# Kernel tuning notes

Measured on AMD Instinct MI355X. Metric: run time of the kernel, lower is better.

## Reference

```python
import jax, jax.numpy as jnp
import numpy as np

B, N, D = 16, 1369, 1024
HID, NH = 512, 8
SCALE = np.sqrt(D // NH)


def _pos_encoding_2d(n, d):
    ps = int(np.sqrt(n))  # 37; n is a perfect square here
    div = jnp.exp(jnp.arange(0, d // 2, 2, dtype=jnp.float32) * (-np.log(10000.0) / (d // 2)))
    rows = (jnp.arange(n) // ps).astype(jnp.float32)
    cols = (jnp.arange(n) % ps).astype(jnp.float32)
    def interleave(s, c):
        return jnp.stack([s, c], axis=-1).reshape(n, -1)
    half_row = interleave(jnp.sin(rows[:, None] * div), jnp.cos(rows[:, None] * div))
    half_col = interleave(jnp.sin(cols[:, None] * div), jnp.cos(cols[:, None] * div))
    return jnp.concatenate([half_row, half_col], axis=-1)  # [n, d]


def _center_bias(n, strength=0.3):
    ps = int(np.sqrt(n))
    c = ps // 2
    y, x = jnp.meshgrid(jnp.arange(ps, dtype=jnp.float32), jnp.arange(ps, dtype=jnp.float32), indexing='ij')
    d2 = (x - c) ** 2 + (y - c) ** 2
    sigma = ps / 6.0
    return (jnp.exp(-d2 / (2.0 * sigma ** 2)).reshape(-1)) * strength  # [n]


def setup_inputs() -> dict:
    key = jax.random.key(0)
    ks = jax.random.split(key, 16)
    s = 0.02
    return {
        'patch_tokens': jax.random.normal(ks[0], (B, N, D), dtype=jnp.float32),
        'curiosity_score': jax.random.uniform(ks[1], (B,), dtype=jnp.float32),
        'Wq': jax.random.normal(ks[2], (D, D), dtype=jnp.float32) * s,
        'bq': jax.random.uniform(ks[3], (D,), minval=-0.05, maxval=0.05, dtype=jnp.float32),
        'Wk': jax.random.normal(ks[4], (D, D), dtype=jnp.float32) * s,
        'bk': jax.random.uniform(ks[5], (D,), minval=-0.05, maxval=0.05, dtype=jnp.float32),
        'Wv': jax.random.normal(ks[6], (D, D), dtype=jnp.float32) * s,
        'bv': jnp.zeros((D,), dtype=jnp.float32),
        'Wc1': jax.random.normal(ks[7], (1, HID // 8), dtype=jnp.float32) * s,
        'bc1': jnp.zeros((HID // 8,), dtype=jnp.float32),
        'Wc2': jax.random.normal(ks[8], (HID // 8, NH), dtype=jnp.float32) * s,
        'bc2': jnp.zeros((NH,), dtype=jnp.float32),
        'Wp1': jax.random.normal(ks[9], (D, HID), dtype=jnp.float32) * s,
        'bp1': jnp.zeros((HID,), dtype=jnp.float32),
        'Wp2': jax.random.normal(ks[10], (HID, HID // 4), dtype=jnp.float32) * s,
        'bp2': jnp.zeros((HID // 4,), dtype=jnp.float32),
        'adaptive_weight': jnp.float32(0.5),
    }


def reference(patch_tokens, curiosity_score, Wq, bq, Wk, bk, Wv, bv,
              Wc1, bc1, Wc2, bc2, Wp1, bp1, Wp2, bp2, adaptive_weight):
    b, n, d = patch_tokens.shape
    x = patch_tokens + _pos_encoding_2d(n, d)[None]  # [B,N,D]

    q = x @ Wq + bq
    k = x @ Wk + bk
    v = x @ Wv + bv

    scores = jnp.einsum('bqd,bkd->bqk', q, k) / SCALE          # [B,N,N]
    attn = jax.nn.softmax(scores, axis=-1)                     # dropout p=0 / eval
    attended = jnp.einsum('bqk,bkd->bqd', attn, v)             # [B,N,D]

    cb = _center_bias(n)[None]                                 # [1,N]
    VAR_EPS = 1e-6

    pa = attn.mean(axis=1) + cb
    # fallback chain (data-dependent in torch; expressed with jnp.where)
    pa2 = jnp.diagonal(attn, axis1=-2, axis2=-1) + cb
    pa = jnp.where(jnp.var(pa, ddof=1) < VAR_EPS, pa2, pa)
    pa3 = attn.max(axis=-1) + cb
    pa = jnp.where(jnp.var(pa, ddof=1) < VAR_EPS, pa3, pa)
    norms = jnp.linalg.norm(x, axis=-1)
    noise = jax.random.normal(jax.random.key(42), norms.shape, dtype=norms.dtype) * 0.1 * jnp.std(norms, ddof=1)
    pa = jnp.where(jnp.var(pa, ddof=1) < VAR_EPS, norms + noise, pa)

    pa = pa / (pa.sum(axis=-1, keepdims=True) + 1e-8)

    # curiosity modulation
    h = jax.nn.relu(curiosity_score[:, None] @ Wc1 + bc1)
    cm = jax.nn.sigmoid(h @ Wc2 + bc2)                         # [B,NH]
    cw = cm.mean(axis=-1, keepdims=True)                       # [B,1]
    modulated = pa * (1.0 + cw)
    fa = adaptive_weight * modulated + (1.0 - adaptive_weight) * pa

    fa = jnp.clip(fa, 1e-8, None)
    fa = fa / (fa.sum(axis=-1, keepdims=True) + 1e-8)

    weighted = jnp.sum(attended * fa[..., None], axis=1)       # [B,D]
    focal = jax.nn.relu(weighted @ Wp1 + bp1) @ Wp2 + bp2      # [B,HID//4]
    return focal, fa
```

## Files before the change

kernel.cpp:

```cpp
#include <hip/hip_runtime.h>
#include <hip/hip_bf16.h>
#include <cstdint>

#define B_   16
#define N_   1369
#define NP   1536
#define D_   1024
#define NQKV 3072
#define SLD  1568
#define QLD  3104

typedef __bf16 bf16x8_t __attribute__((ext_vector_type(8)));
typedef __bf16 bf16x4_t __attribute__((ext_vector_type(4)));
typedef float  f32x4_t  __attribute__((ext_vector_type(4)));

__device__ __forceinline__ float  bf2f(__bf16 x) { return (float)x; }
__device__ __forceinline__ __bf16 f2bf(float x)  { return (__bf16)x; }

#define GLOAD_LDS16(g, l) __builtin_amdgcn_global_load_lds( \
    (const __attribute__((address_space(1))) void*)(g),     \
    (__attribute__((address_space(3))) void*)(l), 16, 0, 0)

__global__ __launch_bounds__(256)
void pos_kernel(float* __restrict__ pos)
{
    const int idx = blockIdx.x * 256 + threadIdx.x;
    if (idx >= N_ * D_) return;
    const int n = idx >> 10, f = idx & 1023;
    const int row = n / 37, col = n - row * 37;
    const float base = (f < 512) ? (float)row : (float)col;
    const int  t2   = (f & 511) >> 1;
    const float dv  = __expf(-0.03597789207803197f * (float)t2);
    const float ang = base * dv;
    pos[idx] = (f & 1) ? cosf(ang) : sinf(ang);
}

__global__ __launch_bounds__(256)
void addpos_kernel(const float* __restrict__ patch, const float* __restrict__ pos,
                   __bf16* __restrict__ X)
{
    const long tid = (long)blockIdx.x * 256 + threadIdx.x;
    const long e   = tid * 4;
    const int  f   = (int)(e & 1023);
    const long nb  = e >> 10;
    const int  n   = (int)(nb % NP);
    const long b   = nb / NP;
    bf16x4_t o;
    if (n < N_) {
        const float4 p = *(const float4*)(patch + ((b * N_ + n) << 10) + f);
        const float4 q = *(const float4*)(pos + ((long)n << 10) + f);
        o[0] = f2bf(p.x + q.x); o[1] = f2bf(p.y + q.y);
        o[2] = f2bf(p.z + q.z); o[3] = f2bf(p.w + q.w);
    } else {
        o[0] = o[1] = o[2] = o[3] = f2bf(0.f);
    }
    *(bf16x4_t*)(X + e) = o;
}

__global__ __launch_bounds__(256)
void wcast_kernel(const float* __restrict__ W0, const float* __restrict__ W1,
                  const float* __restrict__ W2,
                  __bf16* __restrict__ T0, __bf16* __restrict__ T1, __bf16* __restrict__ T2)
{
    const float* W = blockIdx.z == 0 ? W0 : (blockIdx.z == 1 ? W1 : W2);
    __bf16*      T = blockIdx.z == 0 ? T0 : (blockIdx.z == 1 ? T1 : T2);
    __shared__ float tile[64][65];
    const int o0 = blockIdx.x * 64, i0 = blockIdx.y * 64;
    const int t = threadIdx.x;
    const int tr = t >> 4, tc = (t & 15) * 4;
    #pragma unroll
    for (int rr = 0; rr < 64; rr += 16) {
        float4 v = *(const float4*)(W + (long)(i0 + rr + tr) * 1024 + o0 + tc);
        tile[rr + tr][tc + 0] = v.x; tile[rr + tr][tc + 1] = v.y;
        tile[rr + tr][tc + 2] = v.z; tile[rr + tr][tc + 3] = v.w;
    }
    __syncthreads();
    #pragma unroll
    for (int rr = 0; rr < 64; rr += 16) {
        bf16x4_t o;
        o[0] = f2bf(tile[tc + 0][rr + tr]); o[1] = f2bf(tile[tc + 1][rr + tr]);
        o[2] = f2bf(tile[tc + 2][rr + tr]); o[3] = f2bf(tile[tc + 3][rr + tr]);
        *(bf16x4_t*)(T + (long)(o0 + rr + tr) * 1024 + i0 + tc) = o;
    }
}

__global__ __launch_bounds__(256)
void bcat_kernel(const float* __restrict__ bq, const float* __restrict__ bk,
                 const float* __restrict__ bv, float* __restrict__ bcat)
{
    const int i = blockIdx.x * 256 + threadIdx.x;
    if (i >= NQKV) return;
    const int p = i >> 10, j = i & 1023;
    bcat[i] = p == 0 ? bq[j] : (p == 1 ? bk[j] : bv[j]);
}

template<int HAS_BIAS>
__global__ __launch_bounds__(512, 2)
void gemm256(const __bf16* __restrict__ A, const __bf16* __restrict__ Bt,
             __bf16* __restrict__ C, const float* __restrict__ bias,
             int lda, int ldb, int ldc, int Kd, float scale,
             long sA, long sB, long sC, int tilesN, int tilesPerBatch, int cpx)
{
    __shared__ __bf16 lds[65536];
    const int bid = blockIdx.x;
    const int vt  = (bid & 7) * cpx + (bid >> 3);
    const int bz  = vt / tilesPerBatch;
    const int rem = vt - bz * tilesPerBatch;
    const int ty  = rem / tilesN;
    const int tx  = rem - ty * tilesN;
    A  += (long)bz * sA;  Bt += (long)bz * sB;  C += (long)bz * sC;
    const int m0 = ty * 256, n0 = tx * 256;

    const int t  = threadIdx.x;
    const int w  = t >> 6, l = t & 63;
    const int wr = w >> 2, wc = w & 3;
    const int lr = l & 15, lh = l >> 4;

    const int laneF  = (lr * 64 + ((lh * 16) ^ (((lr >> 3) & 1) << 5))) >> 1;
    const int rstage = w * 16 + (l >> 2);
    const int kstage = ((l & 3) * 8) ^ (((l >> 5) & 1) << 4);

    const __bf16* Ag = A  + (long)(m0 + rstage) * lda + kstage;
    const __bf16* Bg = Bt + (long)(n0 + rstage) * ldb + kstage;
    __bf16* dA = lds + (w * 2) * 512;
    __bf16* dB = lds + 16384 + (w * 2) * 512;

#define SA_(buf, half, kt) do {                                       \
    const __bf16* g_ = Ag + (long)(half) * 128 * lda + (kt) * 64;     \
    __bf16* d_ = dA + (buf) * 32768 + (half) * 8192;                  \
    GLOAD_LDS16(g_, d_); GLOAD_LDS16(g_ + 32, d_ + 512); } while (0)
#define SB_(buf, half, kt) do {                                       \
    const __bf16* g_ = Bg + (long)(half) * 128 * ldb + (kt) * 64;     \
    __bf16* d_ = dB + (buf) * 32768 + (half) * 8192;                  \
    GLOAD_LDS16(g_, d_); GLOAD_LDS16(g_ + 32, d_ + 512); } while (0)

    f32x4_t acc[8][4] = {};
    bf16x8_t bfr[4][2];

#define BREADS_() do { const __bf16* bp_ = lds + cbB + laneF;                              \
    bfr[0][0] = *(const bf16x8_t*)(bp_);        bfr[0][1] = *(const bf16x8_t*)(bp_ + 512); \
    bfr[1][0] = *(const bf16x8_t*)(bp_ + 1024); bfr[1][1] = *(const bf16x8_t*)(bp_ + 1536);\
    bfr[2][0] = *(const bf16x8_t*)(bp_ + 2048); bfr[2][1] = *(const bf16x8_t*)(bp_ + 2560);\
    bfr[3][0] = *(const bf16x8_t*)(bp_ + 3072); bfr[3][1] = *(const bf16x8_t*)(bp_ + 3584);} while (0)

#define PHASE_(p, P0R, STG, VMW) do {                                                  \
    const __bf16* ap_ = lds + cbase + wr * 8192 + (p) * 2048 + laneF;                  \
    bf16x8_t a00 = *(const bf16x8_t*)(ap_);                                            \
    bf16x8_t a01 = *(const bf16x8_t*)(ap_ + 512);                                      \
    bf16x8_t a10 = *(const bf16x8_t*)(ap_ + 1024);                                     \
    bf16x8_t a11 = *(const bf16x8_t*)(ap_ + 1536);                                     \
    P0R;                                                                               \
    STG;                                                                               \
    __builtin_amdgcn_s_barrier();                                                      \
    asm volatile("s_waitcnt lgkmcnt(0)" ::: "memory");                                 \
    __builtin_amdgcn_sched_barrier(0);                                                 \
    __builtin_amdgcn_s_setprio(1);                                                     \
    _Pragma("unroll") for (int nn = 0; nn < 4; ++nn)                                   \
      acc[(p)*2+0][nn] = __builtin_amdgcn_mfma_f32_16x16x32_bf16(a00, bfr[nn][0], acc[(p)*2+0][nn], 0, 0, 0); \
    _Pragma("unroll") for (int nn = 0; nn < 4; ++nn)                                   \
      acc[(p)*2+1][nn] = __builtin_amdgcn_mfma_f32_16x16x32_bf16(a10, bfr[nn][0], acc[(p)*2+1][nn], 0, 0, 0); \
    _Pragma("unroll") for (int nn = 0; nn < 4; ++nn)                                   \
      acc[(p)*2+0][nn] = __builtin_amdgcn_mfma_f32_16x16x32_bf16(a01, bfr[nn][1], acc[(p)*2+0][nn], 0, 0, 0); \
    _Pragma("unroll") for (int nn = 0; nn < 4; ++nn)                                   \
      acc[(p)*2+1][nn] = __builtin_amdgcn_mfma_f32_16x16x32_bf16(a11, bfr[nn][1], acc[(p)*2+1][nn], 0, 0, 0); \
    __builtin_amdgcn_s_setprio(0);                                                     \
    VMW;                                                                               \
    __builtin_amdgcn_s_barrier();                                                      \
  } while (0)

    const int NT = Kd >> 6;
    SA_(0, 0, 0); SA_(0, 1, 0); SB_(0, 0, 0); SB_(0, 1, 0);
    SB_(1, 0, 1); SB_(1, 1, 1);
    asm volatile("s_waitcnt vmcnt(4)" ::: "memory");
    __builtin_amdgcn_s_barrier();

    for (int tk = 0; tk < NT; ++tk) {
        const int c  = tk & 1, o = c ^ 1;
        const int t1 = (tk + 1 < NT) ? tk + 1 : NT - 1;
        const int t2 = (tk + 2 < NT) ? tk + 2 : NT - 1;
        const int cbase = c * 32768;
        const int cbB   = cbase + 16384 + wc * 4096;
        PHASE_(0, BREADS_(), SA_(o, 0, t1), ((void)0));
        PHASE_(1, ((void)0), SA_(o, 1, t1), ((void)0));
        PHASE_(2, ((void)0), SB_(c, 0, t2), ((void)0));
        PHASE_(3, ((void)0), SB_(c, 1, t2),
               asm volatile("s_waitcnt vmcnt(4)" ::: "memory"));
    }

    #pragma unroll
    for (int mi = 0; mi < 8; ++mi) {
        const int row = m0 + wr * 128 + mi * 16 + lh * 4;
        #pragma unroll
        for (int nn = 0; nn < 4; ++nn) {
            const int col = n0 + wc * 64 + nn * 16 + lr;
            const float bb = HAS_BIAS ? bias[col] : 0.0f;
            #pragma unroll
            for (int q = 0; q < 4; ++q)
                C[(long)(row + q) * ldc + col] = f2bf(acc[mi][nn][q] * scale + bb);
        }
    }
#undef SA_
#undef SB_
#undef BREADS_
#undef PHASE_
}

__global__ __launch_bounds__(256)
void softmax_kernel(__bf16* __restrict__ S)
{
    const int wid  = threadIdx.x >> 6;
    const int lane = threadIdx.x & 63;
    const int q    = blockIdx.x * 4 + wid;
    const int b    = blockIdx.y;
    if (q >= N_) return;
    __bf16* row = S + ((long)b * NP + q) * SLD;
    float v[24];
    float m = -1e30f;
    #pragma unroll
    for (int j = 0; j < 3; ++j) {
        const int k0 = j * 512 + lane * 8;
        bf16x8_t raw = *(const bf16x8_t*)(row + k0);
        #pragma unroll
        for (int i = 0; i < 8; ++i) {
            const float x = (k0 + i < N_) ? bf2f(raw[i]) : -1e30f;
            v[j * 8 + i] = x; m = fmaxf(m, x);
        }
    }
    #pragma unroll
    for (int o = 32; o; o >>= 1) m = fmaxf(m, __shfl_xor(m, o));
    float s = 0.f;
    #pragma unroll
    for (int j = 0; j < 3; ++j) {
        const int k0 = j * 512 + lane * 8;
        #pragma unroll
        for (int i = 0; i < 8; ++i) {
            if (k0 + i < N_) { const float e = __expf(v[j * 8 + i] - m); v[j * 8 + i] = e; s += e; }
            else             v[j * 8 + i] = 0.f;
        }
    }
    #pragma unroll
    for (int o = 32; o; o >>= 1) s += __shfl_xor(s, o);
    const float inv = 1.f / s;
    #pragma unroll
    for (int j = 0; j < 3; ++j) {
        const int k0 = j * 512 + lane * 8;
        bf16x8_t o8;
        #pragma unroll
        for (int i = 0; i < 8; ++i) o8[i] = f2bf(v[j * 8 + i] * inv);
        *(bf16x8_t*)(row + k0) = o8;
    }
}

template<int WEIGHTED>
__global__ __launch_bounds__(256)
void colsum_kernel(const __bf16* __restrict__ attn, const float* __restrict__ wv,
                   float* __restrict__ out)
{
    const int t = threadIdx.x;
    if (t >= 192) return;
    const int b  = blockIdx.y;
    const int q0 = blockIdx.x * 16;
    const int q1 = (q0 + 16 < N_) ? q0 + 16 : N_;
    const int k8 = t * 8;
    float s[8] = {};
    const __bf16* base = attn + (long)b * NP * SLD + k8;
    for (int q = q0; q < q1; ++q) {
        bf16x8_t v = *(const bf16x8_t*)(base + (long)q * SLD);
        const float wq = WEIGHTED ? wv[b * NP + q] : 1.0f;
        #pragma unroll
        for (int i = 0; i < 8; ++i) s[i] += wq * bf2f(v[i]);
    }
    #pragma unroll
    for (int i = 0; i < 8; ++i) atomicAdd(out + b * NP + k8 + i, s[i]);
}

__global__ __launch_bounds__(256)
void fa_kernel(const float* __restrict__ pa_raw, const float* __restrict__ curiosity,
               const float* __restrict__ Wc1, const float* __restrict__ bc1,
               const float* __restrict__ Wc2, const float* __restrict__ bc2,
               const float* __restrict__ aw_p,
               float* __restrict__ fa_ws, float* __restrict__ out_fa)
{
    const int b = blockIdx.x, t = threadIdx.x;
    __shared__ float hsh[64];
    __shared__ float red[8];
    __shared__ float cwsh;
    if (t < 64) hsh[t] = fmaxf(0.f, curiosity[b] * Wc1[t] + bc1[t]);
    __syncthreads();
    if (t < 8) {
        float a = bc2[t];
        for (int j = 0; j < 64; ++j) a += hsh[j] * Wc2[j * 8 + t];
        red[t] = 1.f / (1.f + __expf(-a));
    }
    __syncthreads();
    if (t == 0) {
        float cw = 0.f;
        for (int i = 0; i < 8; ++i) cw += red[i];
        cwsh = cw * 0.125f;
    }
    __syncthreads();
    const float aw   = aw_p[0];
    const float modf = 1.f + aw * cwsh;
    const float sig  = 37.f / 6.f;
    const float inv2s2 = 1.f / (2.f * sig * sig);
    float pv[6];
    float s1 = 0.f;
    #pragma unroll
    for (int i = 0; i < 6; ++i) {
        const int k = t + i * 256;
        float p = 0.f;
        if (k < N_) {
            const int y = k / 37, x = k - y * 37;
            const float d2 = (float)((x - 18) * (x - 18) + (y - 18) * (y - 18));
            const float cb = 0.3f * __expf(-d2 * inv2s2);
            p = pa_raw[b * NP + k] * (1.f / 1369.f) + cb;
        }
        pv[i] = p; s1 += p;
    }
    #pragma unroll
    for (int o = 32; o; o >>= 1) s1 += __shfl_xor(s1, o);
    __syncthreads();
    if (!(t & 63)) red[t >> 6] = s1;
    __syncthreads();
    s1 = red[0] + red[1] + red[2] + red[3];
    const float inv1 = 1.f / (s1 + 1e-8f);
    float s2 = 0.f;
    #pragma unroll
    for (int i = 0; i < 6; ++i) {
        const int k = t + i * 256;
        if (k < N_) {
            const float f = fmaxf(pv[i] * inv1 * modf, 1e-8f);
            pv[i] = f; s2 += f;
        }
    }
    #pragma unroll
    for (int o = 32; o; o >>= 1) s2 += __shfl_xor(s2, o);
    if (!(t & 63)) red[4 + (t >> 6)] = s2;
    __syncthreads();
    s2 = red[4] + red[5] + red[6] + red[7];
    const float inv2 = 1.f / (s2 + 1e-8f);
    #pragma unroll
    for (int i = 0; i < 6; ++i) {
        const int k = t + i * 256;
        if (k < N_) {
            const float f = pv[i] * inv2;
            fa_ws[b * NP + k]  = f;
            out_fa[b * N_ + k] = f;
        }
    }
}

__global__ __launch_bounds__(256)
void weighted_kernel(const float* __restrict__ g, const __bf16* __restrict__ V,
                     int ldv, float* __restrict__ wout)
{
    const int b  = blockIdx.y;
    const int k0 = blockIdx.x * 86;
    const int k1 = (k0 + 86 < N_) ? k0 + 86 : N_;
    const int d  = threadIdx.x * 4;
    float a0 = 0, a1 = 0, a2 = 0, a3 = 0;
    const __bf16* vb = V + (long)b * NP * ldv + d;
    for (int k = k0; k < k1; ++k) {
        const float gv = g[b * NP + k];
        bf16x4_t vv = *(const bf16x4_t*)(vb + (long)k * ldv);
        a0 += gv * bf2f(vv[0]); a1 += gv * bf2f(vv[1]);
        a2 += gv * bf2f(vv[2]); a3 += gv * bf2f(vv[3]);
    }
    atomicAdd(wout + b * D_ + d + 0, a0);
    atomicAdd(wout + b * D_ + d + 1, a1);
    atomicAdd(wout + b * D_ + d + 2, a2);
    atomicAdd(wout + b * D_ + d + 3, a3);
}

__global__ __launch_bounds__(256)
void focal_kernel(const float* __restrict__ weighted, const float* __restrict__ Wp1,
                  const float* __restrict__ bp1, const float* __restrict__ Wp2,
                  const float* __restrict__ bp2, float* __restrict__ out)
{
    const int b = blockIdx.x, t = threadIdx.x;
    __shared__ float wsh[1024];
    __shared__ float hsh[512];
    for (int i = t; i < 1024; i += 256) wsh[i] = weighted[b * 1024 + i];
    __syncthreads();
    for (int j = t; j < 512; j += 256) {
        float a = bp1[j];
        for (int d2 = 0; d2 < 1024; ++d2) a += wsh[d2] * Wp1[d2 * 512 + j];
        hsh[j] = fmaxf(a, 0.f);
    }
    __syncthreads();
    for (int o = t; o < 128; o += 256) {
        float a = bp2[o];
        for (int j = 0; j < 512; ++j) a += hsh[j] * Wp2[j * 128 + o];
        out[b * 128 + o] = a;
    }
}

extern "C" void kernel_launch(void* const* d_in, const int* in_sizes, int n_in,
                              void* d_out, int out_size, void* d_ws, size_t ws_size,
                              hipStream_t stream)
{
    const float* patch     = (const float*)d_in[0];
    const float* curiosity = (const float*)d_in[1];
    const float* Wq  = (const float*)d_in[2];
    const float* bq  = (const float*)d_in[3];
    const float* Wk  = (const float*)d_in[4];
    const float* bk  = (const float*)d_in[5];
    const float* Wv  = (const float*)d_in[6];
    const float* bv  = (const float*)d_in[7];
    const float* Wc1 = (const float*)d_in[8];
    const float* bc1 = (const float*)d_in[9];
    const float* Wc2 = (const float*)d_in[10];
    const float* bc2 = (const float*)d_in[11];
    const float* Wp1 = (const float*)d_in[12];
    const float* bp1 = (const float*)d_in[13];
    const float* Wp2 = (const float*)d_in[14];
    const float* bp2 = (const float*)d_in[15];
    const float* aw  = (const float*)d_in[16];
    float* out = (float*)d_out;

    char* ws = (char*)d_ws;
    size_t off = 0;
    auto alloc = [&](size_t bytes) -> char* {
        char* p = ws + off;
        off += (bytes + 255) & ~(size_t)255;
        return p;
    };
    float*  pos  = (float*) alloc((size_t)N_ * D_ * 4);
    __bf16* X    = (__bf16*)alloc((size_t)B_ * NP * D_ * 2);
    __bf16* WT   = (__bf16*)alloc((size_t)3 * D_ * D_ * 2);
    const size_t S_BYTES = (size_t)B_ * NP * SLD * 2;
    if (off < S_BYTES) off = S_BYTES;
    __bf16* S    = (__bf16*)ws;
    __bf16* QKV  = (__bf16*)alloc((size_t)B_ * NP * QLD * 2);
    float*  pa   = (float*) alloc((size_t)B_ * NP * 4);
    float*  faw  = (float*) alloc((size_t)B_ * NP * 4);
    float*  gbuf = (float*) alloc((size_t)B_ * NP * 4);
    float*  wsum = (float*) alloc((size_t)B_ * D_ * 4);
    float*  bcat = (float*) alloc((size_t)NQKV * 4);

    (void)hipMemsetAsync(pa,   0, (size_t)B_ * NP * 4, stream);
    (void)hipMemsetAsync(gbuf, 0, (size_t)B_ * NP * 4, stream);
    (void)hipMemsetAsync(wsum, 0, (size_t)B_ * D_ * 4, stream);

    pos_kernel<<<(N_ * D_ + 255) / 256, 256, 0, stream>>>(pos);
    addpos_kernel<<<(int)((size_t)B_ * NP * D_ / 4 / 256), 256, 0, stream>>>(patch, pos, X);
    {
        dim3 g(16, 16, 3);
        wcast_kernel<<<g, 256, 0, stream>>>(Wq, Wk, Wv,
                                            WT, WT + D_ * D_, WT + 2 * D_ * D_);
    }
    bcat_kernel<<<(NQKV + 255) / 256, 256, 0, stream>>>(bq, bk, bv, bcat);
    {
        const int nwg = 96 * 12;
        gemm256<1><<<nwg, 512, 0, stream>>>(X, WT, QKV, bcat,
                                            D_, D_, QLD, D_, 1.0f,
                                            0, 0, 0, 12, nwg, nwg / 8);
    }
    {
        const int nwg = 36 * B_;
        gemm256<0><<<nwg, 512, 0, stream>>>(QKV, QKV + D_, S, nullptr,
                                            QLD, QLD, SLD, D_,
                                            0.08838834764831845f,
                                            (long)NP * QLD, (long)NP * QLD,
                                            (long)NP * SLD, 6, 36, nwg / 8);
    }
    {
        dim3 g((N_ + 3) / 4, B_);
        softmax_kernel<<<g, 256, 0, stream>>>(S);
    }
    {
        dim3 g(86, B_);
        colsum_kernel<0><<<g, 256, 0, stream>>>(S, nullptr, pa);
    }
    fa_kernel<<<B_, 256, 0, stream>>>(pa, curiosity, Wc1, bc1, Wc2, bc2, aw,
                                      faw, out + B_ * 128);
    {
        dim3 g(86, B_);
        colsum_kernel<1><<<g, 256, 0, stream>>>(S, faw, gbuf);
    }
    {
        dim3 g(16, B_);
        weighted_kernel<<<g, 256, 0, stream>>>(gbuf, QKV + 2 * D_, QLD, wsum);
    }
    focal_kernel<<<B_, 256, 0, stream>>>(wsum, Wp1, bp1, Wp2, bp2, out);
}
```

Baseline: 599.5 us.

## Software-pipeline LDS fragment reads in GEMM and split focal MLP into parallel kernels

```diff
diff --git a/kernel.cpp b/kernel.cpp
--- a/kernel.cpp
+++ b/kernel.cpp
@@ -122,8 +122,8 @@
 
     const __bf16* Ag = A  + (long)(m0 + rstage) * lda + kstage;
     const __bf16* Bg = Bt + (long)(n0 + rstage) * ldb + kstage;
-    __bf16* dA = lds + (w * 2) * 512;
-    __bf16* dB = lds + 16384 + (w * 2) * 512;
+    __bf16* dA = lds + w * 1024;
+    __bf16* dB = lds + 16384 + w * 1024;
 
 #define SA_(buf, half, kt) do {                                       \
     const __bf16* g_ = Ag + (long)(half) * 128 * lda + (kt) * 64;     \
@@ -136,55 +136,73 @@
 
     f32x4_t acc[8][4] = {};
     bf16x8_t bfr[4][2];
-
-#define BREADS_() do { const __bf16* bp_ = lds + cbB + laneF;                              \
+    bf16x8_t aX0, aX1, aX2, aX3, aY0, aY1, aY2, aY3;
+
+#define AREAD_(S0,S1,S2,S3, base, p) do {                                    \
+    const __bf16* ap_ = lds + (base) + wr * 8192 + (p) * 2048 + laneF;       \
+    S0 = *(const bf16x8_t*)(ap_);                                            \
+    S1 = *(const bf16x8_t*)(ap_ + 512);                                      \
+    S2 = *(const bf16x8_t*)(ap_ + 1024);                                     \
+    S3 = *(const bf16x8_t*)(ap_ + 1536); } while (0)
+
+#define BREAD_(base) do { const __bf16* bp_ = lds + (base) + laneF;                        \
     bfr[0][0] = *(const bf16x8_t*)(bp_);        bfr[0][1] = *(const bf16x8_t*)(bp_ + 512); \
     bfr[1][0] = *(const bf16x8_t*)(bp_ + 1024); bfr[1][1] = *(const bf16x8_t*)(bp_ + 1536);\
     bfr[2][0] = *(const bf16x8_t*)(bp_ + 2048); bfr[2][1] = *(const bf16x8_t*)(bp_ + 2560);\
     bfr[3][0] = *(const bf16x8_t*)(bp_ + 3072); bfr[3][1] = *(const bf16x8_t*)(bp_ + 3584);} while (0)
 
-#define PHASE_(p, P0R, STG, VMW) do {                                                  \
-    const __bf16* ap_ = lds + cbase + wr * 8192 + (p) * 2048 + laneF;                  \
-    bf16x8_t a00 = *(const bf16x8_t*)(ap_);                                            \
-    bf16x8_t a01 = *(const bf16x8_t*)(ap_ + 512);                                      \
-    bf16x8_t a10 = *(const bf16x8_t*)(ap_ + 1024);                                     \
-    bf16x8_t a11 = *(const bf16x8_t*)(ap_ + 1536);                                     \
-    P0R;                                                                               \
-    STG;                                                                               \
-    __builtin_amdgcn_s_barrier();                                                      \
-    asm volatile("s_waitcnt lgkmcnt(0)" ::: "memory");                                 \
-    __builtin_amdgcn_sched_barrier(0);                                                 \
+#define MFMAC_(pp, S0,S1,S2,S3) do {                                                   \
     __builtin_amdgcn_s_setprio(1);                                                     \
     _Pragma("unroll") for (int nn = 0; nn < 4; ++nn)                                   \
-      acc[(p)*2+0][nn] = __builtin_amdgcn_mfma_f32_16x16x32_bf16(a00, bfr[nn][0], acc[(p)*2+0][nn], 0, 0, 0); \
+      acc[(pp)*2+0][nn] = __builtin_amdgcn_mfma_f32_16x16x32_bf16(S0, bfr[nn][0], acc[(pp)*2+0][nn], 0, 0, 0); \
     _Pragma("unroll") for (int nn = 0; nn < 4; ++nn)                                   \
-      acc[(p)*2+1][nn] = __builtin_amdgcn_mfma_f32_16x16x32_bf16(a10, bfr[nn][0], acc[(p)*2+1][nn], 0, 0, 0); \
+      acc[(pp)*2+1][nn] = __builtin_amdgcn_mfma_f32_16x16x32_bf16(S2, bfr[nn][0], acc[(pp)*2+1][nn], 0, 0, 0); \
     _Pragma("unroll") for (int nn = 0; nn < 4; ++nn)                                   \
-      acc[(p)*2+0][nn] = __builtin_amdgcn_mfma_f32_16x16x32_bf16(a01, bfr[nn][1], acc[(p)*2+0][nn], 0, 0, 0); \
+      acc[(pp)*2+0][nn] = __builtin_amdgcn_mfma_f32_16x16x32_bf16(S1, bfr[nn][1], acc[(pp)*2+0][nn], 0, 0, 0); \
     _Pragma("unroll") for (int nn = 0; nn < 4; ++nn)                                   \
-      acc[(p)*2+1][nn] = __builtin_amdgcn_mfma_f32_16x16x32_bf16(a11, bfr[nn][1], acc[(p)*2+1][nn], 0, 0, 0); \
-    __builtin_amdgcn_s_setprio(0);                                                     \
-    VMW;                                                                               \
-    __builtin_amdgcn_s_barrier();                                                      \
-  } while (0)
+      acc[(pp)*2+1][nn] = __builtin_amdgcn_mfma_f32_16x16x32_bf16(S3, bfr[nn][1], acc[(pp)*2+1][nn], 0, 0, 0); \
+    __builtin_amdgcn_s_setprio(0); } while (0)
+
+#define SBAR_ __builtin_amdgcn_sched_barrier(0)
+#define BAR_  __builtin_amdgcn_s_barrier()
 
     const int NT = Kd >> 6;
     SA_(0, 0, 0); SA_(0, 1, 0); SB_(0, 0, 0); SB_(0, 1, 0);
     SB_(1, 0, 1); SB_(1, 1, 1);
     asm volatile("s_waitcnt vmcnt(4)" ::: "memory");
-    __builtin_amdgcn_s_barrier();
+    BAR_;
 
     for (int tk = 0; tk < NT; ++tk) {
         const int c  = tk & 1, o = c ^ 1;
         const int t1 = (tk + 1 < NT) ? tk + 1 : NT - 1;
         const int t2 = (tk + 2 < NT) ? tk + 2 : NT - 1;
+        const int st = (tk + 2 < NT);
         const int cbase = c * 32768;
         const int cbB   = cbase + 16384 + wc * 4096;
-        PHASE_(0, BREADS_(), SA_(o, 0, t1), ((void)0));
-        PHASE_(1, ((void)0), SA_(o, 1, t1), ((void)0));
-        PHASE_(2, ((void)0), SB_(c, 0, t2), ((void)0));
-        PHASE_(3, ((void)0), SB_(c, 1, t2),
-               asm volatile("s_waitcnt vmcnt(4)" ::: "memory"));
+        AREAD_(aX0, aX1, aX2, aX3, cbase, 0);
+        BREAD_(cbB);
+        SBAR_;
+        AREAD_(aY0, aY1, aY2, aY3, cbase, 1);
+        SA_(o, 0, t1);
+        SBAR_; BAR_;
+        MFMAC_(0, aX0, aX1, aX2, aX3);
+        BAR_;
+        AREAD_(aX0, aX1, aX2, aX3, cbase, 2);
+        SA_(o, 1, t1);
+        SBAR_; BAR_;
+        MFMAC_(1, aY0, aY1, aY2, aY3);
+        BAR_;
+        AREAD_(aY0, aY1, aY2, aY3, cbase, 3);
+        SB_(c, 0, t2);
+        SBAR_; BAR_;
+        MFMAC_(2, aX0, aX1, aX2, aX3);
+        BAR_;
+        SB_(c, 1, t2);
+        SBAR_; BAR_;
+        MFMAC_(3, aY0, aY1, aY2, aY3);
+        if (st) { asm volatile("s_waitcnt vmcnt(4)" ::: "memory"); }
+        else    { asm volatile("s_waitcnt vmcnt(0)" ::: "memory"); }
+        BAR_;
     }
 
     #pragma unroll
@@ -201,8 +219,11 @@
     }
 #undef SA_
 #undef SB_
-#undef BREADS_
-#undef PHASE_
+#undef AREAD_
+#undef BREAD_
+#undef MFMAC_
+#undef SBAR_
+#undef BAR_
 }
 
 __global__ __launch_bounds__(256)
@@ -373,26 +394,35 @@
 }
 
 __global__ __launch_bounds__(256)
-void focal_kernel(const float* __restrict__ weighted, const float* __restrict__ Wp1,
-                  const float* __restrict__ bp1, const float* __restrict__ Wp2,
-                  const float* __restrict__ bp2, float* __restrict__ out)
-{
-    const int b = blockIdx.x, t = threadIdx.x;
-    __shared__ float wsh[1024];
-    __shared__ float hsh[512];
-    for (int i = t; i < 1024; i += 256) wsh[i] = weighted[b * 1024 + i];
-    __syncthreads();
-    for (int j = t; j < 512; j += 256) {
-        float a = bp1[j];
-        for (int d2 = 0; d2 < 1024; ++d2) a += wsh[d2] * Wp1[d2 * 512 + j];
-        hsh[j] = fmaxf(a, 0.f);
-    }
-    __syncthreads();
-    for (int o = t; o < 128; o += 256) {
-        float a = bp2[o];
-        for (int j = 0; j < 512; ++j) a += hsh[j] * Wp2[j * 128 + o];
-        out[b * 128 + o] = a;
-    }
+void focal1_kernel(const float* __restrict__ weighted, const float* __restrict__ Wp1,
+                   const float* __restrict__ bp1, float* __restrict__ h)
+{
+    const int b = blockIdx.y, jc = blockIdx.x;
+    const int t = threadIdx.x;
+    const int jl = t >> 2, part = t & 3;
+    const int j = jc * 64 + jl;
+    const float* wb = weighted + b * 1024 + part * 256;
+    const float* wp = Wp1 + (long)(part * 256) * 512 + j;
+    float a = 0.f;
+    #pragma unroll 8
+    for (int d = 0; d < 256; ++d) a += wb[d] * wp[(long)d * 512];
+    a += __shfl_xor(a, 1);
+    a += __shfl_xor(a, 2);
+    if (part == 0) h[b * 512 + j] = fmaxf(a + bp1[j], 0.f);
+}
+
+__global__ __launch_bounds__(128)
+void focal2_kernel(const float* __restrict__ h, const float* __restrict__ Wp2,
+                   const float* __restrict__ bp2, float* __restrict__ out)
+{
+    const int b = blockIdx.x, o = threadIdx.x;
+    __shared__ float hs[512];
+    for (int i = o; i < 512; i += 128) hs[i] = h[b * 512 + i];
+    __syncthreads();
+    float a = bp2[o];
+    #pragma unroll 8
+    for (int j = 0; j < 512; ++j) a += hs[j] * Wp2[j * 128 + o];
+    out[b * 128 + o] = a;
 }
 
 extern "C" void kernel_launch(void* const* d_in, const int* in_sizes, int n_in,
@@ -437,6 +467,7 @@
     float*  gbuf = (float*) alloc((size_t)B_ * NP * 4);
     float*  wsum = (float*) alloc((size_t)B_ * D_ * 4);
     float*  bcat = (float*) alloc((size_t)NQKV * 4);
+    float*  hbuf = (float*) alloc((size_t)B_ * 512 * 4);
 
     (void)hipMemsetAsync(pa,   0, (size_t)B_ * NP * 4, stream);
     (void)hipMemsetAsync(gbuf, 0, (size_t)B_ * NP * 4, stream);
@@ -482,5 +513,9 @@
         dim3 g(16, B_);
         weighted_kernel<<<g, 256, 0, stream>>>(gbuf, QKV + 2 * D_, QLD, wsum);
     }
-    focal_kernel<<<B_, 256, 0, stream>>>(wsum, Wp1, bp1, Wp2, bp2, out);
-}
+    {
+        dim3 g(8, B_);
+        focal1_kernel<<<g, 256, 0, stream>>>(wsum, Wp1, bp1, hbuf);
+    }
+    focal2_kernel<<<B_, 128, 0, stream>>>(hbuf, Wp2, bp2, out);
+}
```

New measurement: 562.2 us. 6.2% less time.
